# Kernel tuning notes

Hardware: AMD Instinct MI355X
Metric: run time of the kernel (lower is better)

The kernel has to match this reference:

```python
import jax, jax.numpy as jnp
import numpy as np

N = 512          # atoms
MAX_DIST = 16    # shortest-path truncation
N_HEADS = 32
N_SPATIAL = 64
BOND_TYPES = 32  # bond_types_number global in original repo


def setup_inputs() -> dict:
    key = jax.random.key(0)
    k1, k2, k3, k4, k5 = jax.random.split(key, 5)
    spatial_pos = jax.random.randint(k1, (N, N), 0, N_SPATIAL, dtype=jnp.int32)
    edge_input = jax.random.randint(k2, (N, N, MAX_DIST), 0, BOND_TYPES, dtype=jnp.int32)
    # embedding tables; padding_idx=0 -> zero row 0
    spd_table = jax.random.normal(k3, (N_SPATIAL, N_HEADS), dtype=jnp.float32).at[0].set(0.0)
    edge_table = jax.random.normal(k4, (BOND_TYPES, N_HEADS), dtype=jnp.float32).at[0].set(0.0)
    edge_dis_weight = jax.random.normal(k5, (N_SPATIAL * N_HEADS * N_HEADS, 1), dtype=jnp.float32)
    return {
        "spatial_pos": spatial_pos,
        "edge_input": edge_input,
        "max_dist": MAX_DIST,
        "spd_table": spd_table,
        "edge_table": edge_table,
        "edge_dis_weight": edge_dis_weight,
    }


def reference(spatial_pos, edge_input, max_dist, spd_table, edge_table, edge_dis_weight):
    n_heads = spd_table.shape[1]
    # phi_spd: embedding gather [n,n,H] -> [H,n,n]
    phi_spd = jnp.transpose(spd_table[spatial_pos], (2, 0, 1))
    # edge embedding gather: [n,n,D,H]
    edge_emb = edge_table[edge_input]
    # per-distance HxH weight matrices: [D,H,H]
    W = edge_dis_weight.reshape(-1, n_heads, n_heads)[:max_dist]
    # fused per-hop bmm + sum over hops: sum_d edge_emb[i,j,d,:] @ W[d]  -> [n,n,H]
    edge_sum = jnp.einsum('ijdh,dhk->ijk', edge_emb, W)
    # divide by clamped shortest-path distance (0 -> 1)
    denom = jnp.where(spatial_pos == 0, 1, spatial_pos).astype(edge_sum.dtype)[..., None]
    phi_edge = jnp.transpose(edge_sum / denom, (2, 0, 1))
    return (phi_spd, phi_edge)
```

## Files before the change

kernel.cpp:

```cpp
#include <hip/hip_runtime.h>
#include <stdint.h>

#define NH 32

__device__ __forceinline__ float bf_to_f(uint16_t u)
{
    return __uint_as_float(((uint32_t)u) << 16);
}

__device__ __forceinline__ int block_detect_fp32(const uint16_t* p16, int tid,
                                                 int* s_flag)
{
    if (tid == 0) *s_flag = 0;
    __syncthreads();
    const ushort4* p = (const ushort4*)p16;
    ushort4 a = p[tid * 2];
    ushort4 b = p[tid * 2 + 1];
    int big = 0;
    big |= (((a.x >> 7) & 0xFF) >= 0x89); big |= (((a.y >> 7) & 0xFF) >= 0x89);
    big |= (((a.z >> 7) & 0xFF) >= 0x89); big |= (((a.w >> 7) & 0xFF) >= 0x89);
    big |= (((b.x >> 7) & 0xFF) >= 0x89); big |= (((b.y >> 7) & 0xFF) >= 0x89);
    big |= (((b.z >> 7) & 0xFF) >= 0x89); big |= (((b.w >> 7) & 0xFF) >= 0x89);
    if (big) atomicOr(s_flag, 1);
    __syncthreads();
    return *s_flag;
}

__global__ __launch_bounds__(256) void prep(
    const void* __restrict__ edge_table,
    const void* __restrict__ W,
    const void* __restrict__ spd,
    float* __restrict__ T,
    float* __restrict__ spdf,
    int totalT, int spd_n)
{
    __shared__ int s_flag;
    const int tid = threadIdx.x;
    const int is_fp32 = block_detect_fp32((const uint16_t*)spd, tid, &s_flag);
    int g = blockIdx.x * 256 + tid;
    if (g < totalT) {
        int d = g >> 10, e = (g >> 5) & 31, k = g & 31;
        float acc = 0.f;
        if (is_fp32) {
            const float* et = (const float*)edge_table + e * NH;
            const float* w  = (const float*)W + d * NH * NH + k;
#pragma unroll
            for (int h = 0; h < NH; ++h) acc += et[h] * w[h * NH];
        } else {
            const uint16_t* et = (const uint16_t*)edge_table + e * NH;
            const uint16_t* w  = (const uint16_t*)W + d * NH * NH + k;
#pragma unroll
            for (int h = 0; h < NH; ++h) acc += bf_to_f(et[h]) * bf_to_f(w[h * NH]);
        }
        T[g] = acc;
    } else {
        int i = g - totalT;
        if (i < spd_n)
            spdf[i] = is_fp32 ? ((const float*)spd)[i]
                              : bf_to_f(((const uint16_t*)spd)[i]);
    }
}

__device__ __forceinline__ void nt_store2(float* p, float x, float y)
{
    union { float2 f; double d; } u;
    u.f = make_float2(x, y);
    __builtin_nontemporal_store(u.d, (double*)p);
}

__global__ __launch_bounds__(256, 2) void bond2d(
    const int* __restrict__ spatial,
    const int* __restrict__ edge,
    const float* __restrict__ spd_f32,
    const float4* __restrict__ Tg,
    float* __restrict__ out,
    int npairs, int D)
{
    __shared__ float4 Tl[4096];

    const int t     = threadIdx.x;
    const int pw    = blockIdx.x * 256 + t;
    const int base0 = 2 * pw;
    const bool valid = (base0 + 1 < npairs);
    const int base  = valid ? base0 : 0;

    int2 ss = *(const int2*)(spatial + base);

    float acc0[32], acc1[32];
#pragma unroll
    for (int k = 0; k < 32; ++k) { acc0[k] = 0.f; acc1[k] = 0.f; }

    for (int c0 = 0; c0 < D; c0 += 16) {
        const int dlen = (D - c0 < 16) ? (D - c0) : 16;
        __syncthreads();
        if (dlen == 16) {
#pragma unroll
            for (int i = 0; i < 16; ++i) {
                int q = t + i * 256;
                float4 v = Tg[c0 * 256 + q];
                int e    = (q >> 3) & 31;
                int slot = (q & ~7) | ((q & 7) ^ (e & 7));
                Tl[slot] = v;
            }
        } else {
            for (int i = t; i < dlen * 256; i += 256) {
                float4 v = Tg[c0 * 256 + i];
                int e    = (i >> 3) & 31;
                int slot = (i & ~7) | ((i & 7) ^ (e & 7));
                Tl[slot] = v;
            }
        }
        const int* r0 = edge + (size_t)(base + 0) * D + c0;
        const int* r1 = edge + (size_t)(base + 1) * D + c0;

        if (dlen == 16) {
            int4 q0 = ((const int4*)r0)[0], q1 = ((const int4*)r0)[1];
            int4 q2 = ((const int4*)r0)[2], q3 = ((const int4*)r0)[3];
            int4 q4 = ((const int4*)r1)[0], q5 = ((const int4*)r1)[1];
            int4 q6 = ((const int4*)r1)[2], q7 = ((const int4*)r1)[3];
            int e0[16], e1[16];
            e0[0]=q0.x; e0[1]=q0.y; e0[2]=q0.z; e0[3]=q0.w;
            e0[4]=q1.x; e0[5]=q1.y; e0[6]=q1.z; e0[7]=q1.w;
            e0[8]=q2.x; e0[9]=q2.y; e0[10]=q2.z; e0[11]=q2.w;
            e0[12]=q3.x; e0[13]=q3.y; e0[14]=q3.z; e0[15]=q3.w;
            e1[0]=q4.x; e1[1]=q4.y; e1[2]=q4.z; e1[3]=q4.w;
            e1[4]=q5.x; e1[5]=q5.y; e1[6]=q5.z; e1[7]=q5.w;
            e1[8]=q6.x; e1[9]=q6.y; e1[10]=q6.z; e1[11]=q6.w;
            e1[12]=q7.x; e1[13]=q7.y; e1[14]=q7.z; e1[15]=q7.w;
            __syncthreads();
#pragma unroll
            for (int d = 0; d < 16; ++d) {
                {
                    int e = e0[d];
                    int boff = (d << 12) + (e << 7) + ((e & 7) << 4);
#pragma unroll
                    for (int m = 0; m < 8; ++m) {
                        float4 v = *(const float4*)((const char*)Tl + (boff ^ (m << 4)));
                        acc0[4*m+0] += v.x; acc0[4*m+1] += v.y;
                        acc0[4*m+2] += v.z; acc0[4*m+3] += v.w;
                    }
                }
                {
                    int e = e1[d];
                    int boff = (d << 12) + (e << 7) + ((e & 7) << 4);
#pragma unroll
                    for (int m = 0; m < 8; ++m) {
                        float4 v = *(const float4*)((const char*)Tl + (boff ^ (m << 4)));
                        acc1[4*m+0] += v.x; acc1[4*m+1] += v.y;
                        acc1[4*m+2] += v.z; acc1[4*m+3] += v.w;
                    }
                }
            }
        } else {
            int e0[16], e1[16];
            for (int d = 0; d < dlen; ++d) { e0[d] = r0[d]; e1[d] = r1[d]; }
            __syncthreads();
            for (int d = 0; d < dlen; ++d) {
                {
                    int e = e0[d];
                    int boff = (d << 12) + (e << 7) + ((e & 7) << 4);
#pragma unroll
                    for (int m = 0; m < 8; ++m) {
                        float4 v = *(const float4*)((const char*)Tl + (boff ^ (m << 4)));
                        acc0[4*m+0] += v.x; acc0[4*m+1] += v.y;
                        acc0[4*m+2] += v.z; acc0[4*m+3] += v.w;
                    }
                }
                {
                    int e = e1[d];
                    int boff = (d << 12) + (e << 7) + ((e & 7) << 4);
#pragma unroll
                    for (int m = 0; m < 8; ++m) {
                        float4 v = *(const float4*)((const char*)Tl + (boff ^ (m << 4)));
                        acc1[4*m+0] += v.x; acc1[4*m+1] += v.y;
                        acc1[4*m+2] += v.z; acc1[4*m+3] += v.w;
                    }
                }
            }
        }
    }

    if (!valid) return;

    float r0f = 1.0f / (ss.x ? (float)ss.x : 1.0f);
    float r1f = 1.0f / (ss.y ? (float)ss.y : 1.0f);
    float* o1 = out + (size_t)NH * npairs;
#pragma unroll
    for (int k = 0; k < 32; ++k)
        nt_store2(o1 + (size_t)k * npairs + base0, acc0[k] * r0f, acc1[k] * r1f);

    const float* rA = spd_f32 + ss.x * NH;
    const float* rB = spd_f32 + ss.y * NH;
#pragma unroll
    for (int h = 0; h < 32; ++h)
        nt_store2(out + (size_t)h * npairs + base0, rA[h], rB[h]);
}

extern "C" void kernel_launch(void* const* d_in, const int* in_sizes, int n_in,
                              void* d_out, int out_size, void* d_ws, size_t ws_size,
                              hipStream_t stream) {
    const int* spatial = (const int*)d_in[0];
    const int* edge    = (const int*)d_in[1];
    const void* spd    = d_in[3];
    const void* etab   = d_in[4];
    const void* W      = d_in[5];

    long long npairs = in_sizes[0];
    long long etot   = in_sizes[1];
    int D = (int)(etot / (npairs > 0 ? npairs : 1));
    if (D < 1) D = 1;
    if (D > 64) D = 64;
    int spd_n  = in_sizes[3];
    int totalT = D * 1024;

    float* T    = (float*)d_ws;
    float* spdf = T + totalT;

    prep<<<(totalT + spd_n + 255) / 256, 256, 0, stream>>>(
        etab, W, spd, T, spdf, totalT, spd_n);

    int nblk = (int)((npairs + 511) / 512);
    bond2d<<<nblk, 256, 0, stream>>>(spatial, edge, spdf, (const float4*)T,
                                     (float*)d_out, (int)npairs, D);
}
```

Before: 119.7 us.

## Store precomputed edge-weight table in fp16 and drop nontemporal output stores

```diff
diff --git a/kernel.cpp b/kernel.cpp
--- a/kernel.cpp
+++ b/kernel.cpp
@@ -1,4 +1,5 @@
 #include <hip/hip_runtime.h>
+#include <hip/hip_fp16.h>
 #include <stdint.h>
 
 #define NH 32
@@ -30,7 +31,7 @@
     const void* __restrict__ edge_table,
     const void* __restrict__ W,
     const void* __restrict__ spd,
-    float* __restrict__ T,
+    __half* __restrict__ T16,
     float* __restrict__ spdf,
     int totalT, int spd_n)
 {
@@ -52,7 +53,7 @@
 #pragma unroll
             for (int h = 0; h < NH; ++h) acc += bf_to_f(et[h]) * bf_to_f(w[h * NH]);
         }
-        T[g] = acc;
+        T16[g] = __float2half(acc);
     } else {
         int i = g - totalT;
         if (i < spd_n)
@@ -61,22 +62,26 @@
     }
 }
 
-__device__ __forceinline__ void nt_store2(float* p, float x, float y)
-{
-    union { float2 f; double d; } u;
-    u.f = make_float2(x, y);
-    __builtin_nontemporal_store(u.d, (double*)p);
+__device__ __forceinline__ void acc8(float* acc, uint4 v)
+{
+    const __half2* h = (const __half2*)&v;
+    float2 f0 = __half22float2(h[0]);
+    float2 f1 = __half22float2(h[1]);
+    float2 f2 = __half22float2(h[2]);
+    float2 f3 = __half22float2(h[3]);
+    acc[0] += f0.x; acc[1] += f0.y; acc[2] += f1.x; acc[3] += f1.y;
+    acc[4] += f2.x; acc[5] += f2.y; acc[6] += f3.x; acc[7] += f3.y;
 }
 
 __global__ __launch_bounds__(256, 2) void bond2d(
     const int* __restrict__ spatial,
     const int* __restrict__ edge,
     const float* __restrict__ spd_f32,
-    const float4* __restrict__ Tg,
+    const uint4* __restrict__ Tg16,
     float* __restrict__ out,
     int npairs, int D)
 {
-    __shared__ float4 Tl[4096];
+    __shared__ uint4 Tl[2048];
 
     const int t     = threadIdx.x;
     const int pw    = blockIdx.x * 256 + t;
@@ -92,22 +97,25 @@
 
     for (int c0 = 0; c0 < D; c0 += 16) {
         const int dlen = (D - c0 < 16) ? (D - c0) : 16;
+        const int nch  = dlen * 128;
         __syncthreads();
         if (dlen == 16) {
 #pragma unroll
-            for (int i = 0; i < 16; ++i) {
+            for (int i = 0; i < 8; ++i) {
                 int q = t + i * 256;
-                float4 v = Tg[c0 * 256 + q];
-                int e    = (q >> 3) & 31;
-                int slot = (q & ~7) | ((q & 7) ^ (e & 7));
-                Tl[slot] = v;
+                uint4 v = Tg16[c0 * 128 + q];
+                int d = q >> 7, e = (q >> 2) & 31, m = q & 3;
+                int slot = (d << 11) + ((e >> 1) << 7)
+                         + (((((e & 1) << 2) | m) ^ ((e >> 1) & 7)) << 4);
+                *(uint4*)((char*)Tl + slot) = v;
             }
         } else {
-            for (int i = t; i < dlen * 256; i += 256) {
-                float4 v = Tg[c0 * 256 + i];
-                int e    = (i >> 3) & 31;
-                int slot = (i & ~7) | ((i & 7) ^ (e & 7));
-                Tl[slot] = v;
+            for (int q = t; q < nch; q += 256) {
+                uint4 v = Tg16[c0 * 128 + q];
+                int d = q >> 7, e = (q >> 2) & 31, m = q & 3;
+                int slot = (d << 11) + ((e >> 1) << 7)
+                         + (((((e & 1) << 2) | m) ^ ((e >> 1) & 7)) << 4);
+                *(uint4*)((char*)Tl + slot) = v;
             }
         }
         const int* r0 = edge + (size_t)(base + 0) * D + c0;
@@ -132,22 +140,22 @@
             for (int d = 0; d < 16; ++d) {
                 {
                     int e = e0[d];
-                    int boff = (d << 12) + (e << 7) + ((e & 7) << 4);
-#pragma unroll
-                    for (int m = 0; m < 8; ++m) {
-                        float4 v = *(const float4*)((const char*)Tl + (boff ^ (m << 4)));
-                        acc0[4*m+0] += v.x; acc0[4*m+1] += v.y;
-                        acc0[4*m+2] += v.z; acc0[4*m+3] += v.w;
+                    int boff = (d << 11) + ((e >> 1) << 7)
+                             + ((((e & 1) << 2) ^ ((e >> 1) & 7)) << 4);
+#pragma unroll
+                    for (int m = 0; m < 4; ++m) {
+                        uint4 v = *(const uint4*)((const char*)Tl + (boff ^ (m << 4)));
+                        acc8(&acc0[8 * m], v);
                     }
                 }
                 {
                     int e = e1[d];
-                    int boff = (d << 12) + (e << 7) + ((e & 7) << 4);
-#pragma unroll
-                    for (int m = 0; m < 8; ++m) {
-                        float4 v = *(const float4*)((const char*)Tl + (boff ^ (m << 4)));
-                        acc1[4*m+0] += v.x; acc1[4*m+1] += v.y;
-                        acc1[4*m+2] += v.z; acc1[4*m+3] += v.w;
+                    int boff = (d << 11) + ((e >> 1) << 7)
+                             + ((((e & 1) << 2) ^ ((e >> 1) & 7)) << 4);
+#pragma unroll
+                    for (int m = 0; m < 4; ++m) {
+                        uint4 v = *(const uint4*)((const char*)Tl + (boff ^ (m << 4)));
+                        acc8(&acc1[8 * m], v);
                     }
                 }
             }
@@ -158,22 +166,22 @@
             for (int d = 0; d < dlen; ++d) {
                 {
                     int e = e0[d];
-                    int boff = (d << 12) + (e << 7) + ((e & 7) << 4);
-#pragma unroll
-                    for (int m = 0; m < 8; ++m) {
-                        float4 v = *(const float4*)((const char*)Tl + (boff ^ (m << 4)));
-                        acc0[4*m+0] += v.x; acc0[4*m+1] += v.y;
-                        acc0[4*m+2] += v.z; acc0[4*m+3] += v.w;
+                    int boff = (d << 11) + ((e >> 1) << 7)
+                             + ((((e & 1) << 2) ^ ((e >> 1) & 7)) << 4);
+#pragma unroll
+                    for (int m = 0; m < 4; ++m) {
+                        uint4 v = *(const uint4*)((const char*)Tl + (boff ^ (m << 4)));
+                        acc8(&acc0[8 * m], v);
                     }
                 }
                 {
                     int e = e1[d];
-                    int boff = (d << 12) + (e << 7) + ((e & 7) << 4);
-#pragma unroll
-                    for (int m = 0; m < 8; ++m) {
-                        float4 v = *(const float4*)((const char*)Tl + (boff ^ (m << 4)));
-                        acc1[4*m+0] += v.x; acc1[4*m+1] += v.y;
-                        acc1[4*m+2] += v.z; acc1[4*m+3] += v.w;
+                    int boff = (d << 11) + ((e >> 1) << 7)
+                             + ((((e & 1) << 2) ^ ((e >> 1) & 7)) << 4);
+#pragma unroll
+                    for (int m = 0; m < 4; ++m) {
+                        uint4 v = *(const uint4*)((const char*)Tl + (boff ^ (m << 4)));
+                        acc8(&acc1[8 * m], v);
                     }
                 }
             }
@@ -187,13 +195,15 @@
     float* o1 = out + (size_t)NH * npairs;
 #pragma unroll
     for (int k = 0; k < 32; ++k)
-        nt_store2(o1 + (size_t)k * npairs + base0, acc0[k] * r0f, acc1[k] * r1f);
+        *(float2*)(o1 + (size_t)k * npairs + base0) =
+            make_float2(acc0[k] * r0f, acc1[k] * r1f);
 
     const float* rA = spd_f32 + ss.x * NH;
     const float* rB = spd_f32 + ss.y * NH;
 #pragma unroll
     for (int h = 0; h < 32; ++h)
-        nt_store2(out + (size_t)h * npairs + base0, rA[h], rB[h]);
+        *(float2*)(out + (size_t)h * npairs + base0) =
+            make_float2(rA[h], rB[h]);
 }
 
 extern "C" void kernel_launch(void* const* d_in, const int* in_sizes, int n_in,
@@ -213,13 +223,13 @@
     int spd_n  = in_sizes[3];
     int totalT = D * 1024;
 
-    float* T    = (float*)d_ws;
-    float* spdf = T + totalT;
+    __half* T16 = (__half*)d_ws;
+    float*  spdf = (float*)((char*)d_ws + ((size_t)totalT * 2 + 255 & ~255ull));
 
     prep<<<(totalT + spd_n + 255) / 256, 256, 0, stream>>>(
-        etab, W, spd, T, spdf, totalT, spd_n);
+        etab, W, spd, T16, spdf, totalT, spd_n);
 
     int nblk = (int)((npairs + 511) / 512);
-    bond2d<<<nblk, 256, 0, stream>>>(spatial, edge, spdf, (const float4*)T,
+    bond2d<<<nblk, 256, 0, stream>>>(spatial, edge, spdf, (const uint4*)T16,
                                      (float*)d_out, (int)npairs, D);
 }
```

After: 145.1 us. 21.2% more time.
